# Performance work log

Measured on AMD Instinct MI355X. Metric: run time of the kernel, lower is better.

Reference implementation:

```python
import jax, jax.numpy as jnp
import numpy as np

B, S, HID = 2, 2048, 2048
H, KV, D = 16, 4, 128
ROT = 64           # partial rotary dim (= cos.shape[-1])
EMB = 128          # router embedding dim
TAU, BASE = 0.4, 3.0
EPS = 1e-6


def rotate_half(x):
    h = x.shape[-1] // 2
    return jnp.concatenate([-x[..., h:], x[..., :h]], axis=-1)


def rmsnorm(x, w, eps=EPS):
    # Qwen3.5: zero-init weight, (1 + w) scaling, compute in fp32
    xf = x.astype(jnp.float32)
    o = xf * jax.lax.rsqrt(jnp.mean(xf * xf, axis=-1, keepdims=True) + eps)
    return (o * (1.0 + w.astype(jnp.float32))).astype(x.dtype)


def _rope_tables():
    inv_freq = 1.0 / (10000.0 ** (np.arange(0, ROT, 2, dtype=np.float32) / ROT))
    t = np.arange(S, dtype=np.float32)
    freqs = np.outer(t, inv_freq)                 # [S, ROT/2]
    emb = np.concatenate([freqs, freqs], axis=-1)  # [S, ROT]
    cos = np.broadcast_to(np.cos(emb), (B, S, ROT)).copy()
    sin = np.broadcast_to(np.sin(emb), (B, S, ROT)).copy()
    return jnp.asarray(cos), jnp.asarray(sin)


def setup_inputs() -> dict:
    key = jax.random.key(0)
    ks = jax.random.split(key, 10)
    sc = 0.02
    cos, sin = _rope_tables()
    return {
        "hidden_states": jax.random.normal(ks[0], (B, S, HID), jnp.float32),
        "cos": cos,
        "sin": sin,
        # projection weights stored as [in, out] (torch Linear weight transposed)
        "Wq": jax.random.normal(ks[1], (HID, H * D * 2), jnp.float32) * sc,
        "Wk": jax.random.normal(ks[2], (HID, KV * D), jnp.float32) * sc,
        "Wv": jax.random.normal(ks[3], (HID, KV * D), jnp.float32) * sc,
        "Wo": jax.random.normal(ks[4], (H * D, HID), jnp.float32) * sc,
        "q_norm_w": jnp.zeros((D,), jnp.float32),
        "k_norm_w": jnp.zeros((D,), jnp.float32),
        "Wr": jax.random.normal(ks[5], (HID, EMB), jnp.float32) * sc,   # router linear
        "Wd": jax.random.normal(ks[6], (EMB, D), jnp.float32) * sc,     # router decoder
        "ln_g": jnp.ones((EMB,), jnp.float32),
        "ln_b": jnp.zeros((EMB,), jnp.float32),
        "rnn_state": jnp.zeros((EMB,), jnp.float32),
    }


def _forward(hidden_states, cos, sin, Wq, Wk, Wv, Wo, q_norm_w, k_norm_w,
             Wr, Wd, ln_g, ln_b, rnn_state):
    b, s, _ = hidden_states.shape
    # doubled q_proj -> query + gate
    qkv = jnp.einsum('bsh,hd->bsd', hidden_states, Wq).reshape(b, s, H, 2 * D)
    q, gate = qkv[..., :D], qkv[..., D:]
    gate = gate.reshape(b, s, H * D)
    k = jnp.einsum('bsh,hd->bsd', hidden_states, Wk).reshape(b, s, KV, D)
    v = jnp.einsum('bsh,hd->bsd', hidden_states, Wv).reshape(b, s, KV, D)
    # per-head RMSNorm then [b, h, s, d]
    q = rmsnorm(q, q_norm_w).transpose(0, 2, 1, 3)
    k = rmsnorm(k, k_norm_w).transpose(0, 2, 1, 3)
    v = v.transpose(0, 2, 1, 3)

    # --- head-dim router (gumbel-sigmoid, straight-through hard round) ---
    emb = jnp.einsum('bsh,he->bse', hidden_states, Wr) + rnn_state
    mu = jnp.mean(emb, -1, keepdims=True)
    var = jnp.mean((emb - mu) ** 2, -1, keepdims=True)
    ln = (emb - mu) * jax.lax.rsqrt(var + 1e-5) * ln_g + ln_b
    logits = jnp.einsum('bse,ed->bsd', jax.nn.gelu(ln, approximate=False), Wd)
    gum = -jnp.log(jax.random.exponential(jax.random.key(42), logits.shape, jnp.float32))
    y_soft = jax.nn.sigmoid((logits + gum + BASE) / TAU)
    binary = jax.lax.stop_gradient(jnp.round(y_soft) - y_soft) + y_soft  # [b, s, D]
    mask = binary[:, None, :, :]  # broadcast over heads: [b, 1, s, D]

    q = q * mask
    k = k * mask

    # partial RoPE on first ROT dims (qk_index=None training path)
    c = cos[:, None, :, :]
    si = sin[:, None, :, :]
    def rope(x):
        xr, xp = x[..., :ROT], x[..., ROT:]
        return jnp.concatenate([xr * c + rotate_half(xr) * si, xp], axis=-1)
    q = rope(q)
    k = rope(k)

    # GQA: repeat kv heads
    rep = H // KV
    k = jnp.repeat(k, rep, axis=1)
    v = jnp.repeat(v, rep, axis=1)

    scores = jnp.einsum('bhqd,bhkd->bhqk', q, k) / np.sqrt(D).astype(np.float32)
    causal = jnp.tril(jnp.ones((s, s), bool))
    scores = jnp.where(causal, scores, jnp.finfo(jnp.float32).min)
    attn = jax.nn.softmax(scores.astype(jnp.float32), axis=-1).astype(q.dtype)
    out = jnp.einsum('bhqk,bhkd->bhqd', attn, v)
    out = out.transpose(0, 2, 1, 3).reshape(b, s, H * D)
    out = out * jax.nn.sigmoid(gate)   # output gate
    return jnp.einsum('bsd,dh->bsh', out, Wo)


def reference(hidden_states, cos, sin, Wq, Wk, Wv, Wo, q_norm_w, k_norm_w,
              Wr, Wd, ln_g, ln_b, rnn_state):
    return _forward(hidden_states, cos, sin, Wq, Wk, Wv, Wo, q_norm_w, k_norm_w,
                    Wr, Wd, ln_g, ln_b, rnn_state)
```

## Files before the change

kernel.cpp:

```cpp
#include <hip/hip_runtime.h>
#include <math.h>

typedef __bf16 bf16;
typedef bf16 bf16x8 __attribute__((ext_vector_type(8)));
typedef bf16 bf16x4 __attribute__((ext_vector_type(4)));
typedef float f32x4 __attribute__((ext_vector_type(4)));

#define BB 2
#define SS 2048
#define NKVE 1152
#define QSCALE (0.08838834764831845f * 1.4426950408889634f)

__device__ __forceinline__ float waveAllReduceSum(float v) {
#pragma unroll
  for (int o = 1; o < 64; o <<= 1) v += __shfl_xor(v, o, 64);
  return v;
}

__device__ __forceinline__ int xcd_swz(int orig, int nwg) {
  return (orig & 7) * (nwg >> 3) + (orig >> 3);
}

__device__ __forceinline__ void gload16(const bf16* g, bf16* l) {
  __builtin_amdgcn_global_load_lds((const __attribute__((address_space(1))) void*)g,
                                   (__attribute__((address_space(3))) void*)l, 16, 0, 0);
}

__device__ __forceinline__ void do_transpose(bf16 (*tile)[72], const float* __restrict__ W,
                                             bf16* __restrict__ WT, int K, int N, int rowOff,
                                             int bx, int by, int t) {
  int n0 = bx * 64, k0 = by * 64;
  {
    int c4 = (t & 15) * 4, r = t >> 4;
#pragma unroll
    for (int p = 0; p < 4; p++) {
      int row = p * 16 + r;
      float4 v = *reinterpret_cast<const float4*>(W + (size_t)(k0 + row) * N + n0 + c4);
      bf16x4 o = {(bf16)v.x, (bf16)v.y, (bf16)v.z, (bf16)v.w};
      *reinterpret_cast<bf16x4*>(&tile[row][c4]) = o;
    }
  }
  __syncthreads();
  {
    int ln = t & 7, n = t >> 3;
#pragma unroll
    for (int p = 0; p < 2; p++) {
      int nn = p * 32 + n;
      bf16x8 o;
#pragma unroll
      for (int j = 0; j < 8; j++) o[j] = tile[ln * 8 + j][nn];
      *reinterpret_cast<bf16x8*>(WT + (size_t)(rowOff + n0 + nn) * K + k0 + ln * 8) = o;
    }
  }
  __syncthreads();
}

__global__ __launch_bounds__(256) void prep_weights(const float* __restrict__ hidden,
                                                    const float* __restrict__ Wq,
                                                    const float* __restrict__ Wk,
                                                    const float* __restrict__ Wv,
                                                    const float* __restrict__ Wr,
                                                    const float* __restrict__ Wo,
                                                    bf16* __restrict__ hb,
                                                    bf16* __restrict__ WTall,
                                                    bf16* __restrict__ WoT) {
  __shared__ bf16 tile[64][72];
  int id = blockIdx.x, t = threadIdx.x;
  if (id < 4096) {
    int i = (id * 256 + t) * 8;
    float4 v0 = *reinterpret_cast<const float4*>(hidden + i);
    float4 v1 = *reinterpret_cast<const float4*>(hidden + i + 4);
    bf16x8 o = {(bf16)v0.x, (bf16)v0.y, (bf16)v0.z, (bf16)v0.w,
                (bf16)v1.x, (bf16)v1.y, (bf16)v1.z, (bf16)v1.w};
    *reinterpret_cast<bf16x8*>(hb + i) = o;
    return;
  }
  int id2 = id - 4096;
  if (id2 < 2048) { do_transpose(tile, Wq, WTall, 2048, 4096, 0, id2 & 63, id2 >> 6, t); return; }
  id2 -= 2048;
  if (id2 < 256) { do_transpose(tile, Wk, WTall, 2048, 512, 4096, id2 & 7, id2 >> 3, t); return; }
  id2 -= 256;
  if (id2 < 256) { do_transpose(tile, Wv, WTall, 2048, 512, 4608, id2 & 7, id2 >> 3, t); return; }
  id2 -= 256;
  if (id2 < 64) { do_transpose(tile, Wr, WTall, 2048, 128, 5120, id2 & 1, id2 >> 1, t); return; }
  id2 -= 64;
  do_transpose(tile, Wo, WoT, 2048, 2048, 0, id2 & 31, id2 >> 5, t);
}

template <typename CT>
__global__ __launch_bounds__(256) void gemm_bt(const bf16* __restrict__ A,
                                               const bf16* __restrict__ Bt,
                                               CT* __restrict__ C, int M, int N, int K) {
  __shared__ bf16 lA[128 * 64];
  __shared__ bf16 lB[128 * 64];
  const int nbx = N >> 7;
  int wg = xcd_swz(blockIdx.x, gridDim.x);
  int bx = wg % nbx, by = wg / nbx;
  const int t = threadIdx.x;
  const int l = t & 63, w = t >> 6;
  const int wr = w >> 1, wc = w & 1;
  const int lr = l & 15, lhi = l >> 4;

  f32x4 acc[4][4];
#pragma unroll
  for (int m = 0; m < 4; m++)
#pragma unroll
    for (int n = 0; n < 4; n++) acc[m][n] = f32x4{0.f, 0.f, 0.f, 0.f};

  const int rowA0 = by * 128, rowB0 = bx * 128;
  const int nkt = K >> 6;
  for (int kt = 0; kt < nkt; ++kt) {
    __syncthreads();
#pragma unroll
    for (int it = 0; it < 4; ++it) {
      int slot = it * 256 + t;
      int row = slot >> 3, sl = slot & 7;
      gload16(A + (size_t)(rowA0 + row) * K + kt * 64 + ((sl ^ (row & 7)) << 3), lA + slot * 8);
      gload16(Bt + (size_t)(rowB0 + row) * K + kt * 64 + ((sl ^ (row & 7)) << 3), lB + slot * 8);
    }
    __syncthreads();
#pragma unroll
    for (int kc = 0; kc < 2; ++kc) {
      bf16x8 af[4], bg[4];
#pragma unroll
      for (int m = 0; m < 4; m++) {
        int row = wr * 64 + m * 16 + lr;
        af[m] = *reinterpret_cast<const bf16x8*>((char*)lA + row * 128 + (((kc * 4 + lhi) ^ (row & 7)) << 4));
      }
#pragma unroll
      for (int n = 0; n < 4; n++) {
        int row = wc * 64 + n * 16 + lr;
        bg[n] = *reinterpret_cast<const bf16x8*>((char*)lB + row * 128 + (((kc * 4 + lhi) ^ (row & 7)) << 4));
      }
      __builtin_amdgcn_s_setprio(1);
#pragma unroll
      for (int m = 0; m < 4; m++)
#pragma unroll
        for (int n = 0; n < 4; n++)
          acc[m][n] = __builtin_amdgcn_mfma_f32_16x16x32_bf16(af[m], bg[n], acc[m][n], 0, 0, 0);
      __builtin_amdgcn_s_setprio(0);
    }
  }
#pragma unroll
  for (int m = 0; m < 4; m++)
#pragma unroll
    for (int n = 0; n < 4; n++)
#pragma unroll
      for (int r = 0; r < 4; r++) {
        int grow = rowA0 + wr * 64 + m * 16 + lhi * 4 + r;
        int gcol = rowB0 + wc * 64 + n * 16 + lr;
        C[(size_t)grow * N + gcol] = (CT)acc[m][n][r];
      }
}

__global__ __launch_bounds__(512, 2) void gemm_qg(const bf16* __restrict__ A,
                                                  const bf16* __restrict__ Bt,
                                                  bf16* __restrict__ Cq) {
  __shared__ bf16 lA[2][256 * 64];
  __shared__ bf16 lB[2][256 * 64];
  int wg = xcd_swz(blockIdx.x, 256);
  int bx = wg & 15, by = wg >> 4;
  const int t = threadIdx.x;
  const int l = t & 63, w = t >> 6;
  const int wm = w >> 2, wn = w & 3;
  const int lr = l & 15, lhi = l >> 4;
  const int K = 2048;

  f32x4 acc[8][4];
#pragma unroll
  for (int m = 0; m < 8; m++)
#pragma unroll
    for (int n = 0; n < 4; n++) acc[m][n] = f32x4{0.f, 0.f, 0.f, 0.f};

  const int rowA0 = by * 256, rowB0 = bx * 256;

  auto stage = [&](int buf, int kt) {
#pragma unroll
    for (int it = 0; it < 4; ++it) {
      int slot = it * 512 + t;
      int row = slot >> 3, sl = slot & 7;
      gload16(A + (size_t)(rowA0 + row) * K + kt * 64 + ((sl ^ (row & 7)) << 3), lA[buf] + slot * 8);
      gload16(Bt + (size_t)(rowB0 + row) * K + kt * 64 + ((sl ^ (row & 7)) << 3), lB[buf] + slot * 8);
    }
  };

  stage(0, 0);
  stage(1, 1);

  for (int kt = 0; kt < 32; ++kt) {
    int cur = kt & 1;
    if (kt < 31) {
      asm volatile("s_waitcnt vmcnt(8)" ::: "memory");
    } else {
      asm volatile("s_waitcnt vmcnt(0)" ::: "memory");
    }
    __builtin_amdgcn_sched_barrier(0);
    __builtin_amdgcn_s_barrier();
    __builtin_amdgcn_sched_barrier(0);

#pragma unroll
    for (int ks = 0; ks < 2; ++ks) {
      bf16x8 bg[4];
#pragma unroll
      for (int n = 0; n < 4; n++) {
        int row = wn * 64 + n * 16 + lr;
        bg[n] = *reinterpret_cast<const bf16x8*>((char*)lB[cur] + row * 128 + (((ks * 4 + lhi) ^ (row & 7)) << 4));
      }
#pragma unroll
      for (int mh = 0; mh < 2; ++mh) {
        bf16x8 af[4];
#pragma unroll
        for (int m = 0; m < 4; m++) {
          int row = wm * 128 + (mh * 4 + m) * 16 + lr;
          af[m] = *reinterpret_cast<const bf16x8*>((char*)lA[cur] + row * 128 + (((ks * 4 + lhi) ^ (row & 7)) << 4));
        }
        __builtin_amdgcn_s_setprio(1);
#pragma unroll
        for (int m = 0; m < 4; m++)
#pragma unroll
          for (int n = 0; n < 4; n++)
            acc[mh * 4 + m][n] = __builtin_amdgcn_mfma_f32_16x16x32_bf16(af[m], bg[n], acc[mh * 4 + m][n], 0, 0, 0);
        __builtin_amdgcn_s_setprio(0);
      }
    }

    asm volatile("s_waitcnt lgkmcnt(0)" ::: "memory");
    __builtin_amdgcn_sched_barrier(0);
    __builtin_amdgcn_s_barrier();
    __builtin_amdgcn_sched_barrier(0);
    if (kt + 2 < 32) stage(cur, kt + 2);
  }

#pragma unroll
  for (int m = 0; m < 8; m++)
#pragma unroll
    for (int n = 0; n < 4; n++)
#pragma unroll
      for (int r = 0; r < 4; r++) {
        int grow = rowA0 + wm * 128 + m * 16 + lhi * 4 + r;
        int gcol = rowB0 + wn * 64 + n * 16 + lr;
        Cq[(size_t)grow * 4096 + gcol] = (bf16)acc[m][n][r];
      }
}

__global__ __launch_bounds__(512, 2) void gemm_out(const bf16* __restrict__ A,
                                                   const bf16* __restrict__ Bt,
                                                   float* __restrict__ C) {
  __shared__ bf16 lA[2][256 * 64];
  __shared__ bf16 lB[2][128 * 64];
  int wg = xcd_swz(blockIdx.x, 256);
  int bx = wg & 15, by = wg >> 4;
  const int t = threadIdx.x;
  const int l = t & 63, w = t >> 6;
  const int wm = w >> 1, wn = w & 1;
  const int lr = l & 15, lhi = l >> 4;
  const int K = 2048;

  f32x4 acc[4][4];
#pragma unroll
  for (int m = 0; m < 4; m++)
#pragma unroll
    for (int n = 0; n < 4; n++) acc[m][n] = f32x4{0.f, 0.f, 0.f, 0.f};

  const int rowA0 = by * 256, rowB0 = bx * 128;

  auto stage = [&](int buf, int kt) {
#pragma unroll
    for (int it = 0; it < 4; ++it) {
      int slot = it * 512 + t;
      int row = slot >> 3, sl = slot & 7;
      gload16(A + (size_t)(rowA0 + row) * K + kt * 64 + ((sl ^ (row & 7)) << 3), lA[buf] + slot * 8);
    }
#pragma unroll
    for (int it = 0; it < 2; ++it) {
      int slot = it * 512 + t;
      int row = slot >> 3, sl = slot & 7;
      gload16(Bt + (size_t)(rowB0 + row) * K + kt * 64 + ((sl ^ (row & 7)) << 3), lB[buf] + slot * 8);
    }
  };

  stage(0, 0);
  stage(1, 1);

  for (int kt = 0; kt < 32; ++kt) {
    int cur = kt & 1;
    if (kt < 31) {
      asm volatile("s_waitcnt vmcnt(6)" ::: "memory");
    } else {
      asm volatile("s_waitcnt vmcnt(0)" ::: "memory");
    }
    __builtin_amdgcn_sched_barrier(0);
    __builtin_amdgcn_s_barrier();
    __builtin_amdgcn_sched_barrier(0);

#pragma unroll
    for (int ks = 0; ks < 2; ++ks) {
      bf16x8 bg[4];
#pragma unroll
      for (int n = 0; n < 4; n++) {
        int row = wn * 64 + n * 16 + lr;
        bg[n] = *reinterpret_cast<const bf16x8*>((char*)lB[cur] + row * 128 + (((ks * 4 + lhi) ^ (row & 7)) << 4));
      }
      bf16x8 af[4];
#pragma unroll
      for (int m = 0; m < 4; m++) {
        int row = wm * 64 + m * 16 + lr;
        af[m] = *reinterpret_cast<const bf16x8*>((char*)lA[cur] + row * 128 + (((ks * 4 + lhi) ^ (row & 7)) << 4));
      }
      __builtin_amdgcn_s_setprio(1);
#pragma unroll
      for (int m = 0; m < 4; m++)
#pragma unroll
        for (int n = 0; n < 4; n++)
          acc[m][n] = __builtin_amdgcn_mfma_f32_16x16x32_bf16(af[m], bg[n], acc[m][n], 0, 0, 0);
      __builtin_amdgcn_s_setprio(0);
    }

    asm volatile("s_waitcnt lgkmcnt(0)" ::: "memory");
    __builtin_amdgcn_sched_barrier(0);
    __builtin_amdgcn_s_barrier();
    __builtin_amdgcn_sched_barrier(0);
    if (kt + 2 < 32) stage(cur, kt + 2);
  }

#pragma unroll
  for (int m = 0; m < 4; m++)
#pragma unroll
    for (int n = 0; n < 4; n++)
#pragma unroll
      for (int r = 0; r < 4; r++) {
        int grow = rowA0 + wm * 64 + m * 16 + lhi * 4 + r;
        int gcol = rowB0 + wn * 64 + n * 16 + lr;
        C[(size_t)grow * 2048 + gcol] = acc[m][n][r];
      }
}

__device__ __forceinline__ unsigned rotl32(unsigned x, int r) { return (x << r) | (x >> (32 - r)); }

__device__ __forceinline__ float gumbel42(unsigned i) {
  const unsigned half = (unsigned)(BB * SS * 128) / 2u;
  unsigned x0, x1;
  int word;
  if (i < half) { x0 = i; x1 = i + half; word = 0; }
  else          { x0 = i - half; x1 = i; word = 1; }
  const unsigned k0 = 0u, k1 = 42u;
  const unsigned k2 = k0 ^ k1 ^ 0x1BD11BDAu;
  x0 += k0; x1 += k1;
#define TF_R(r) { x0 += x1; x1 = rotl32(x1, r); x1 ^= x0; }
  TF_R(13) TF_R(15) TF_R(26) TF_R(6)
  x0 += k1; x1 += k2 + 1u;
  TF_R(17) TF_R(29) TF_R(16) TF_R(24)
  x0 += k2; x1 += k0 + 2u;
  TF_R(13) TF_R(15) TF_R(26) TF_R(6)
  x0 += k0; x1 += k1 + 3u;
  TF_R(17) TF_R(29) TF_R(16) TF_R(24)
  x0 += k1; x1 += k2 + 4u;
  TF_R(13) TF_R(15) TF_R(26) TF_R(6)
  x0 += k2; x1 += k0 + 5u;
#undef TF_R
  unsigned bits = word ? x1 : x0;
  float u = __uint_as_float((bits >> 9) | 0x3f800000u) - 1.0f;
  float ex = -log1pf(-u);
  return -logf(ex);
}

__global__ __launch_bounds__(128) void mask_kernel(const bf16* __restrict__ kve,
                                                   const float* __restrict__ rnn,
                                                   const float* __restrict__ lng,
                                                   const float* __restrict__ lnb,
                                                   const float* __restrict__ Wd,
                                                   bf16* __restrict__ maskb) {
  int row = blockIdx.x;
  int t = threadIdx.x;
  int l = t & 63, w = t >> 6;
  __shared__ float redm[2], redv[2], gsh[128];
  float e = (float)kve[(size_t)row * NKVE + 1024 + t] + rnn[t];
  float s1 = waveAllReduceSum(e);
  if (l == 0) redm[w] = s1;
  __syncthreads();
  float mu = (redm[0] + redm[1]) * (1.0f / 128.0f);
  float dv = (e - mu) * (e - mu);
  float s2 = waveAllReduceSum(dv);
  if (l == 0) redv[w] = s2;
  __syncthreads();
  float var = (redv[0] + redv[1]) * (1.0f / 128.0f);
  float ln = (e - mu) * rsqrtf(var + 1e-5f) * lng[t] + lnb[t];
  float g = 0.5f * ln * (1.0f + erff(ln * 0.7071067811865475f));
  gsh[t] = g;
  __syncthreads();
  float logit = 0.f;
#pragma unroll 8
  for (int e2 = 0; e2 < 128; e2++) logit += gsh[e2] * Wd[e2 * 128 + t];
  float gum = gumbel42((unsigned)(row * 128 + t));
  float x = (logit + gum + 3.0f) * 2.5f;
  float y = 1.0f / (1.0f + expf(-x));
  maskb[(size_t)row * 128 + t] = (bf16)rintf(y);
}

__global__ __launch_bounds__(256) void qkv_prep(const bf16* __restrict__ kve,
                                                const bf16* __restrict__ maskb,
                                                const float* __restrict__ kw,
                                                const float* __restrict__ cosT,
                                                const float* __restrict__ sinT,
                                                bf16* __restrict__ wk,
                                                bf16* __restrict__ wvt) {
  int id = blockIdx.x, t = threadIdx.x;
  if (id < 1024) {
    int g = t >> 4, ln = t & 15;
    int hr = id * 16 + g;
    int kv = hr & 3, row = hr >> 2;
    int b = row >> 11, s = row & 2047;
    const bf16* kp = kve + (size_t)row * NKVE + kv * 128 + ln * 8;
    bf16x8 k8 = *reinterpret_cast<const bf16x8*>(kp);
    bf16x8 m8 = *reinterpret_cast<const bf16x8*>(maskb + (size_t)row * 128 + ln * 8);
    float kf[8], ss = 0.f;
#pragma unroll
    for (int j = 0; j < 8; j++) { kf[j] = (float)k8[j]; ss += kf[j] * kf[j]; }
#pragma unroll
    for (int o = 1; o < 16; o <<= 1) ss += __shfl_xor(ss, o, 16);
    float rinv = rsqrtf(ss * (1.0f / 128.0f) + 1e-6f);
    alignas(16) float wv[8];
    const float4* kw4 = reinterpret_cast<const float4*>(kw);
    *reinterpret_cast<float4*>(&wv[0]) = kw4[ln * 2];
    *reinterpret_cast<float4*>(&wv[4]) = kw4[ln * 2 + 1];
    float km[8];
#pragma unroll
    for (int j = 0; j < 8; j++) km[j] = kf[j] * rinv * (1.0f + wv[j]) * (float)m8[j];
    alignas(16) float c8[8], s8[8];
    if (ln < 8) {
      const float4* c4 = reinterpret_cast<const float4*>(cosT + (size_t)row * 64);
      const float4* sn4 = reinterpret_cast<const float4*>(sinT + (size_t)row * 64);
      *reinterpret_cast<float4*>(&c8[0]) = c4[ln * 2];
      *reinterpret_cast<float4*>(&c8[4]) = c4[ln * 2 + 1];
      *reinterpret_cast<float4*>(&s8[0]) = sn4[ln * 2];
      *reinterpret_cast<float4*>(&s8[4]) = sn4[ln * 2 + 1];
    }
    float po[8];
#pragma unroll
    for (int j = 0; j < 8; j++) po[j] = __shfl_xor(km[j], 4, 16);
    bf16x8 ok;
#pragma unroll
    for (int j = 0; j < 8; j++) {
      float ov;
      if (ln < 4) ov = km[j] * c8[j] - po[j] * s8[j];
      else if (ln < 8) ov = km[j] * c8[j] + po[j] * s8[j];
      else ov = km[j];
      ok[j] = (bf16)ov;
    }
    *reinterpret_cast<bf16x8*>(wk + ((size_t)((b * 4 + kv) * 2048 + s)) * 128 + ln * 8) = ok;
    return;
  }
  {
    __shared__ bf16 tl[64][72];
    int vb = id - 1024;
    int dt = vb & 1;
    int st = (vb >> 1) & 31;
    int bkv = vb >> 6;
    int b = bkv >> 2, kv = bkv & 3;
    int tx = t & 63, ty = t >> 6;
    int s0 = st * 64, d0 = dt * 64;
#pragma unroll
    for (int i = 0; i < 16; i++) {
      int srow = ty + i * 4;
      tl[srow][tx] = kve[(size_t)(b * 2048 + s0 + srow) * NKVE + 512 + kv * 128 + d0 + tx];
    }
    __syncthreads();
#pragma unroll
    for (int i = 0; i < 16; i++) {
      int drow = ty + i * 4;
      wvt[(size_t)((b * 4 + kv) * 128 + d0 + drow) * 2048 + s0 + tx] = tl[tx][drow];
    }
  }
}

__global__ __launch_bounds__(512) void attn_kernel(const bf16* __restrict__ qg,
                                                   const bf16* __restrict__ wk,
                                                   const bf16* __restrict__ wvt,
                                                   const bf16* __restrict__ maskb,
                                                   const float* __restrict__ qw,
                                                   const float* __restrict__ cosT,
                                                   const float* __restrict__ sinT,
                                                   bf16* __restrict__ wattn) {
  __shared__ bf16 lK[2][64 * 128];
  __shared__ bf16 lV[2][128 * 64];
  __shared__ bf16 lP[8][16 * 64];
  int bid = blockIdx.x;
  int grp = bid & 7;
  int b = grp >> 2, kvh = grp & 3;
  int g32 = bid >> 3;
  int pp = g32 & 7;
  int h = kvh * 4 + (g32 >> 3);
  int bh = b * 16 + h;
  int t = threadIdx.x, l = t & 63, w = t >> 6;
  int lr = l & 15, lhi = l >> 4;

  const bf16* kbase = wk + (size_t)((b * 4 + kvh) * 2048) * 128;
  const bf16* vbase = wvt + (size_t)((b * 4 + kvh) * 128) * 2048;
  char* pb = (char*)(&lP[w][0]);

  const int n0 = 2 * pp + 2;

  int rowK = t >> 4, slK = t & 15;
  const bf16* kp0 = kbase + rowK * 128 + ((slK ^ (rowK & 7)) << 3);
  int rowV = t >> 3, slV = t & 7;
  const bf16* vp0 = vbase + (size_t)rowV * 2048 + ((slV ^ (rowV & 7)) << 3);
  const bf16* kp = kp0;
  const bf16* vp = vp0;

  auto stage = [&](int buf) {
    gload16(kp, lK[buf] + t * 8);
    gload16(kp + 4096, lK[buf] + (512 + t) * 8);
    gload16(vp, lV[buf] + t * 8);
    gload16(vp + 131072, lV[buf] + (512 + t) * 8);
  };

  bf16x8 aq[4];
  f32x4 oacc[8];
  float l_run;
  int qb128 = pp;

  auto load_q = [&](int qbv) {
    int srow = qbv * 128 + w * 16 + lr;
    int grow = b * 2048 + srow;
    const bf16* qp = qg + (size_t)grow * 4096 + h * 256;
    int dbase = lhi * 8;
    float qf[4][8];
    float ss = 0.f;
#pragma unroll
    for (int kc = 0; kc < 4; kc++) {
      bf16x8 v = *reinterpret_cast<const bf16x8*>(qp + kc * 32 + dbase);
#pragma unroll
      for (int j = 0; j < 8; j++) { qf[kc][j] = (float)v[j]; ss += qf[kc][j] * qf[kc][j]; }
    }
    ss += __shfl_xor(ss, 16, 64);
    ss += __shfl_xor(ss, 32, 64);
    float rinv = rsqrtf(ss * (1.0f / 128.0f) + 1e-6f);
    const bf16* mrow = maskb + (size_t)grow * 128;
    float qm[4][8];
#pragma unroll
    for (int kc = 0; kc < 4; kc++) {
      bf16x8 m8 = *reinterpret_cast<const bf16x8*>(mrow + kc * 32 + dbase);
      float4 wa = *reinterpret_cast<const float4*>(qw + kc * 32 + dbase);
      float4 wb = *reinterpret_cast<const float4*>(qw + kc * 32 + dbase + 4);
      alignas(16) float wv[8];
      *reinterpret_cast<float4*>(&wv[0]) = wa;
      *reinterpret_cast<float4*>(&wv[4]) = wb;
#pragma unroll
      for (int j = 0; j < 8; j++) qm[kc][j] = qf[kc][j] * rinv * (1.0f + wv[j]) * (float)m8[j];
    }
    const float* crow = cosT + (size_t)grow * 64;
    const float* srw = sinT + (size_t)grow * 64;
    alignas(16) float c0[8], c1[8], s0[8], s1[8];
    *reinterpret_cast<float4*>(&c0[0]) = *reinterpret_cast<const float4*>(crow + dbase);
    *reinterpret_cast<float4*>(&c0[4]) = *reinterpret_cast<const float4*>(crow + dbase + 4);
    *reinterpret_cast<float4*>(&c1[0]) = *reinterpret_cast<const float4*>(crow + 32 + dbase);
    *reinterpret_cast<float4*>(&c1[4]) = *reinterpret_cast<const float4*>(crow + 32 + dbase + 4);
    *reinterpret_cast<float4*>(&s0[0]) = *reinterpret_cast<const float4*>(srw + dbase);
    *reinterpret_cast<float4*>(&s0[4]) = *reinterpret_cast<const float4*>(srw + dbase + 4);
    *reinterpret_cast<float4*>(&s1[0]) = *reinterpret_cast<const float4*>(srw + 32 + dbase);
    *reinterpret_cast<float4*>(&s1[4]) = *reinterpret_cast<const float4*>(srw + 32 + dbase + 4);
#pragma unroll
    for (int j = 0; j < 8; j++) {
      float o0 = qm[0][j] * c0[j] - qm[1][j] * s0[j];
      float o1 = qm[1][j] * c1[j] + qm[0][j] * s1[j];
      aq[0][j] = (bf16)(o0 * QSCALE);
      aq[1][j] = (bf16)(o1 * QSCALE);
      aq[2][j] = (bf16)(qm[2][j] * QSCALE);
      aq[3][j] = (bf16)(qm[3][j] * QSCALE);
    }
  };

  load_q(pp);
#pragma unroll
  for (int db = 0; db < 8; db++) oacc[db] = f32x4{0.f, 0.f, 0.f, 0.f};
  l_run = 0.f;

  stage(0);
  kp += 8192; vp += 64;
  __syncthreads();
  int cur = 0;

  for (int i = 0; i < 34; ++i) {
    int tt = (i < n0) ? i : i - n0;
    if (i + 1 < 34) {
      if (i + 1 == n0) { kp = kp0; vp = vp0; }
      stage(cur ^ 1);
      kp += 8192; vp += 64;
    }
    int qrow0 = qb128 * 128 + w * 16;

    f32x4 sacc[4];
#pragma unroll
    for (int j = 0; j < 4; j++) sacc[j] = f32x4{0.f, 0.f, 0.f, 0.f};
    __builtin_amdgcn_s_setprio(1);
#pragma unroll
    for (int kc = 0; kc < 4; kc++)
#pragma unroll
      for (int j = 0; j < 4; j++) {
        int row = j * 16 + lr;
        bf16x8 ak = *reinterpret_cast<const bf16x8*>((char*)lK[cur] + row * 256 + (((kc * 4 + lhi) ^ (row & 7)) << 4));
        sacc[j] = __builtin_amdgcn_mfma_f32_16x16x32_bf16(ak, aq[kc], sacc[j], 0, 0, 0);
      }
    __builtin_amdgcn_s_setprio(0);

    if (tt * 64 + 63 > qrow0) {
      int qrow_g = qrow0 + lr;
#pragma unroll
      for (int j = 0; j < 4; j++)
#pragma unroll
        for (int r = 0; r < 4; r++) {
          int kg = tt * 64 + j * 16 + lhi * 4 + r;
          if (kg > qrow_g) sacc[j][r] = -1e30f;
        }
    }

    float p[4][4];
    float sj[4];
#pragma unroll
    for (int j = 0; j < 4; j++) {
#pragma unroll
      for (int r = 0; r < 4; r++) p[j][r] = exp2f(sacc[j][r]);
      sj[j] = (p[j][0] + p[j][1]) + (p[j][2] + p[j][3]);
    }
    l_run += (sj[0] + sj[1]) + (sj[2] + sj[3]);

#pragma unroll
    for (int j = 0; j < 4; j++) {
      bf16x4 p4 = {(bf16)p[j][0], (bf16)p[j][1], (bf16)p[j][2], (bf16)p[j][3]};
      *reinterpret_cast<bf16x4*>(pb + lr * 128 + ((j * 32 + lhi * 8) ^ ((lr & 7) << 4))) = p4;
    }
    bf16x8 pa[2];
#pragma unroll
    for (int kc2 = 0; kc2 < 2; kc2++)
      pa[kc2] = *reinterpret_cast<const bf16x8*>(pb + lr * 128 + ((kc2 * 64 + lhi * 16) ^ ((lr & 7) << 4)));
    __builtin_amdgcn_s_setprio(1);
#pragma unroll
    for (int kc2 = 0; kc2 < 2; kc2++)
#pragma unroll
      for (int db = 0; db < 8; db++) {
        int row = db * 16 + lr;
        bf16x8 bv = *reinterpret_cast<const bf16x8*>((char*)lV[cur] + row * 128 + (((kc2 * 4 + lhi) ^ (row & 7)) << 4));
        oacc[db] = __builtin_amdgcn_mfma_f32_16x16x32_bf16(pa[kc2], bv, oacc[db], 0, 0, 0);
      }
    __builtin_amdgcn_s_setprio(0);

    if (i == n0 - 1 || i == 33) {
      float lsum = l_run;
      lsum += __shfl_xor(lsum, 16, 64);
      lsum += __shfl_xor(lsum, 32, 64);
      float linv[4];
#pragma unroll
      for (int r = 0; r < 4; r++) linv[r] = 1.0f / __shfl(lsum, lhi * 4 + r, 64);
#pragma unroll
      for (int r = 0; r < 4; r++) {
        int srow = qb128 * 128 + w * 16 + lhi * 4 + r;
        const bf16* grow_p = qg + (size_t)(b * 2048 + srow) * 4096 + h * 256 + 128;
#pragma unroll
        for (int db = 0; db < 8; db++) {
          int dcol = db * 16 + lr;
          float graw = (float)grow_p[dcol];
          float g = 1.0f / (1.0f + expf(-graw));
          float ov = oacc[db][r] * linv[r] * g;
          wattn[(size_t)(b * 2048 + srow) * 2048 + h * 128 + dcol] = (bf16)ov;
        }
      }
      if (i == n0 - 1) {
        qb128 = 15 - pp;
        load_q(qb128);
#pragma unroll
        for (int db = 0; db < 8; db++) oacc[db] = f32x4{0.f, 0.f, 0.f, 0.f};
        l_run = 0.f;
      }
    }

    __syncthreads();
    cur ^= 1;
  }
}

extern "C" void kernel_launch(void* const* d_in, const int* in_sizes, int n_in,
                              void* d_out, int out_size, void* d_ws, size_t ws_size,
                              hipStream_t stream) {
  const float* hidden = (const float*)d_in[0];
  const float* cosT = (const float*)d_in[1];
  const float* sinT = (const float*)d_in[2];
  const float* Wq = (const float*)d_in[3];
  const float* Wk = (const float*)d_in[4];
  const float* Wv = (const float*)d_in[5];
  const float* Wo = (const float*)d_in[6];
  const float* qw = (const float*)d_in[7];
  const float* kw = (const float*)d_in[8];
  const float* Wr = (const float*)d_in[9];
  const float* Wd = (const float*)d_in[10];
  const float* lng = (const float*)d_in[11];
  const float* lnb = (const float*)d_in[12];
  const float* rnn = (const float*)d_in[13];
  float* out = (float*)d_out;

  char* p = (char*)d_ws;
  auto alloc = [&](size_t bytes) { char* r = p; p += (bytes + 255) & ~(size_t)255; return r; };
  bf16* hb    = (bf16*)alloc((size_t)4096 * 2048 * 2);
  bf16* WTall = (bf16*)alloc((size_t)5248 * 2048 * 2);
  bf16* WoT   = (bf16*)alloc((size_t)2048 * 2048 * 2);
  bf16* qgb   = (bf16*)alloc((size_t)4096 * 4096 * 2);
  bf16* kveb  = (bf16*)alloc((size_t)4096 * NKVE * 2);
  bf16* maskb = (bf16*)alloc((size_t)4096 * 128 * 2);
  bf16* wkb   = (bf16*)alloc((size_t)2 * 4 * 2048 * 128 * 2);
  bf16* wvtb  = (bf16*)alloc((size_t)2 * 4 * 128 * 2048 * 2);
  bf16* wab   = (bf16*)alloc((size_t)4096 * 2048 * 2);
  if ((size_t)(p - (char*)d_ws) > ws_size) return;

  prep_weights<<<7744, 256, 0, stream>>>(hidden, Wq, Wk, Wv, Wr, Wo, hb, WTall, WoT);

  gemm_bt<bf16><<<288, 256, 0, stream>>>(hb, WTall + (size_t)4096 * 2048, kveb, 4096, NKVE, 2048);

  mask_kernel<<<4096, 128, 0, stream>>>(kveb, rnn, lng, lnb, Wd, maskb);

  gemm_qg<<<256, 512, 0, stream>>>(hb, WTall, qgb);

  qkv_prep<<<1536, 256, 0, stream>>>(kveb, maskb, kw, cosT, sinT, wkb, wvtb);

  attn_kernel<<<256, 512, 0, stream>>>(qgb, wkb, wvtb, maskb, qw, cosT, sinT, wab);

  gemm_out<<<256, 512, 0, stream>>>(wab, WoT, out);
}
```

Measured before the change: 275.2 us.

## Split paired causal q-blocks into separate workgroups, scheduled longest-first

The attention kernel used to have each of 256 workgroups process two 128-row query blocks, pp and 15-pp, back to back so causal work was balanced per block. Now 512 workgroups each handle a single query block, ordered so the longest blocks (15, 13, ...) are dispatched first and the short ones fill in later. This exposes more parallelism on a device with many CUs and removes the mid-loop Q reload and epilogue branch. The cost is per-block imbalance that now depends on the hardware scheduler, plus a duplicated Q-load prologue per workgroup.

Result: slower. 297.2 us (+8.0%).

```diff
diff --git a/kernel.cpp b/kernel.cpp
--- a/kernel.cpp
+++ b/kernel.cpp
@@ -487,9 +487,11 @@
   int bid = blockIdx.x;
   int grp = bid & 7;
   int b = grp >> 2, kvh = grp & 3;
-  int g32 = bid >> 3;
-  int pp = g32 & 7;
-  int h = kvh * 4 + (g32 >> 3);
+  int rest = bid >> 3;
+  int hsub = rest & 3;
+  int qidx = rest >> 2;
+  int qi = (qidx < 8) ? (15 - 2 * qidx) : (2 * (qidx - 8));
+  int h = kvh * 4 + hsub;
   int bh = b * 16 + h;
   int t = threadIdx.x, l = t & 63, w = t >> 6;
   int lr = l & 15, lhi = l >> 4;
@@ -498,29 +500,25 @@
   const bf16* vbase = wvt + (size_t)((b * 4 + kvh) * 128) * 2048;
   char* pb = (char*)(&lP[w][0]);
 
-  const int n0 = 2 * pp + 2;
-
-  int rowK = t >> 4, slK = t & 15;
-  const bf16* kp0 = kbase + rowK * 128 + ((slK ^ (rowK & 7)) << 3);
-  int rowV = t >> 3, slV = t & 7;
-  const bf16* vp0 = vbase + (size_t)rowV * 2048 + ((slV ^ (rowV & 7)) << 3);
-  const bf16* kp = kp0;
-  const bf16* vp = vp0;
-
-  auto stage = [&](int buf) {
-    gload16(kp, lK[buf] + t * 8);
-    gload16(kp + 4096, lK[buf] + (512 + t) * 8);
-    gload16(vp, lV[buf] + t * 8);
-    gload16(vp + 131072, lV[buf] + (512 + t) * 8);
+  const int nkv = 2 * qi + 2;
+
+  auto stage = [&](int buf, int tt) {
+#pragma unroll
+    for (int it = 0; it < 2; ++it) {
+      int slot = it * 512 + t;
+      int row = slot >> 4, sl = slot & 15;
+      gload16(kbase + (size_t)(tt * 64 + row) * 128 + ((sl ^ (row & 7)) << 3), lK[buf] + slot * 8);
+      int row2 = slot >> 3, sl2 = slot & 7;
+      gload16(vbase + (size_t)row2 * 2048 + tt * 64 + ((sl2 ^ (row2 & 7)) << 3), lV[buf] + slot * 8);
+    }
   };
 
   bf16x8 aq[4];
   f32x4 oacc[8];
   float l_run;
-  int qb128 = pp;
-
-  auto load_q = [&](int qbv) {
-    int srow = qbv * 128 + w * 16 + lr;
+
+  {
+    int srow = qi * 128 + w * 16 + lr;
     int grow = b * 2048 + srow;
     const bf16* qp = qg + (size_t)grow * 4096 + h * 256;
     int dbase = lhi * 8;
@@ -540,11 +538,9 @@
 #pragma unroll
     for (int kc = 0; kc < 4; kc++) {
       bf16x8 m8 = *reinterpret_cast<const bf16x8*>(mrow + kc * 32 + dbase);
-      float4 wa = *reinterpret_cast<const float4*>(qw + kc * 32 + dbase);
-      float4 wb = *reinterpret_cast<const float4*>(qw + kc * 32 + dbase + 4);
       alignas(16) float wv[8];
-      *reinterpret_cast<float4*>(&wv[0]) = wa;
-      *reinterpret_cast<float4*>(&wv[4]) = wb;
+      *reinterpret_cast<float4*>(&wv[0]) = *reinterpret_cast<const float4*>(qw + kc * 32 + dbase);
+      *reinterpret_cast<float4*>(&wv[4]) = *reinterpret_cast<const float4*>(qw + kc * 32 + dbase + 4);
 #pragma unroll
       for (int j = 0; j < 8; j++) qm[kc][j] = qf[kc][j] * rinv * (1.0f + wv[j]) * (float)m8[j];
     }
@@ -568,26 +564,19 @@
       aq[2][j] = (bf16)(qm[2][j] * QSCALE);
       aq[3][j] = (bf16)(qm[3][j] * QSCALE);
     }
-  };
-
-  load_q(pp);
+  }
+
 #pragma unroll
   for (int db = 0; db < 8; db++) oacc[db] = f32x4{0.f, 0.f, 0.f, 0.f};
   l_run = 0.f;
 
-  stage(0);
-  kp += 8192; vp += 64;
+  stage(0, 0);
   __syncthreads();
   int cur = 0;
-
-  for (int i = 0; i < 34; ++i) {
-    int tt = (i < n0) ? i : i - n0;
-    if (i + 1 < 34) {
-      if (i + 1 == n0) { kp = kp0; vp = vp0; }
-      stage(cur ^ 1);
-      kp += 8192; vp += 64;
-    }
-    int qrow0 = qb128 * 128 + w * 16;
+  int qrow0 = qi * 128 + w * 16;
+
+  for (int i = 0; i < nkv; ++i) {
+    if (i + 1 < nkv) stage(cur ^ 1, i + 1);
 
     f32x4 sacc[4];
 #pragma unroll
@@ -603,13 +592,13 @@
       }
     __builtin_amdgcn_s_setprio(0);
 
-    if (tt * 64 + 63 > qrow0) {
+    if (i * 64 + 63 > qrow0) {
       int qrow_g = qrow0 + lr;
 #pragma unroll
       for (int j = 0; j < 4; j++)
 #pragma unroll
         for (int r = 0; r < 4; r++) {
-          int kg = tt * 64 + j * 16 + lhi * 4 + r;
+          int kg = i * 64 + j * 16 + lhi * 4 + r;
           if (kg > qrow_g) sacc[j][r] = -1e30f;
         }
     }
@@ -644,37 +633,28 @@
       }
     __builtin_amdgcn_s_setprio(0);
 
-    if (i == n0 - 1 || i == 33) {
-      float lsum = l_run;
-      lsum += __shfl_xor(lsum, 16, 64);
-      lsum += __shfl_xor(lsum, 32, 64);
-      float linv[4];
-#pragma unroll
-      for (int r = 0; r < 4; r++) linv[r] = 1.0f / __shfl(lsum, lhi * 4 + r, 64);
-#pragma unroll
-      for (int r = 0; r < 4; r++) {
-        int srow = qb128 * 128 + w * 16 + lhi * 4 + r;
-        const bf16* grow_p = qg + (size_t)(b * 2048 + srow) * 4096 + h * 256 + 128;
-#pragma unroll
-        for (int db = 0; db < 8; db++) {
-          int dcol = db * 16 + lr;
-          float graw = (float)grow_p[dcol];
-          float g = 1.0f / (1.0f + expf(-graw));
-          float ov = oacc[db][r] * linv[r] * g;
-          wattn[(size_t)(b * 2048 + srow) * 2048 + h * 128 + dcol] = (bf16)ov;
-        }
-      }
-      if (i == n0 - 1) {
-        qb128 = 15 - pp;
-        load_q(qb128);
-#pragma unroll
-        for (int db = 0; db < 8; db++) oacc[db] = f32x4{0.f, 0.f, 0.f, 0.f};
-        l_run = 0.f;
-      }
-    }
-
     __syncthreads();
     cur ^= 1;
+  }
+
+  float lsum = l_run;
+  lsum += __shfl_xor(lsum, 16, 64);
+  lsum += __shfl_xor(lsum, 32, 64);
+  float linv[4];
+#pragma unroll
+  for (int r = 0; r < 4; r++) linv[r] = 1.0f / __shfl(lsum, lhi * 4 + r, 64);
+#pragma unroll
+  for (int r = 0; r < 4; r++) {
+    int srow = qi * 128 + w * 16 + lhi * 4 + r;
+    const bf16* grow_p = qg + (size_t)(b * 2048 + srow) * 4096 + h * 256 + 128;
+#pragma unroll
+    for (int db = 0; db < 8; db++) {
+      int dcol = db * 16 + lr;
+      float graw = (float)grow_p[dcol];
+      float g = 1.0f / (1.0f + expf(-graw));
+      float ov = oacc[db][r] * linv[r] * g;
+      wattn[(size_t)(b * 2048 + srow) * 2048 + h * 128 + dcol] = (bf16)ov;
+    }
   }
 }
 
@@ -720,7 +700,7 @@
 
   qkv_prep<<<1536, 256, 0, stream>>>(kveb, maskb, kw, cosT, sinT, wkb, wvtb);
 
-  attn_kernel<<<256, 512, 0, stream>>>(qgb, wkb, wvtb, maskb, qw, cosT, sinT, wab);
+  attn_kernel<<<512, 512, 0, stream>>>(qgb, wkb, wvtb, maskb, qw, cosT, sinT, wab);
 
   gemm_out<<<256, 512, 0, stream>>>(wab, WoT, out);
 }
```
